# Kernel tuning notes

Measured on AMD Instinct MI355X. Metric: run time of the kernel, lower is better.

Reference implementation:

```python
import jax, jax.numpy as jnp
import numpy as np

B, S, D = 8, 512, 1024
F = 4 * D        # FFN hidden
E = 8            # num experts
SCALE = 0.02


def setup_inputs() -> dict:
    key = jax.random.key(0)
    ks = jax.random.split(key, 16)
    n = lambda k, shape, s=SCALE: (jax.random.normal(k, shape, dtype=jnp.float32) * s)
    task_ids = jax.random.randint(ks[15], (B,), 0, E)
    return {
        "hidden_states": jax.random.normal(ks[0], (B, S, D), dtype=jnp.float32),
        "ohe_task": jax.nn.one_hot(task_ids, E, dtype=jnp.float32),
        # base model (2-layer FFN) params
        "W1": n(ks[1], (D, F)), "b1": n(ks[2], (F,)),
        "W2": n(ks[3], (F, D)), "b2": n(ks[4], (D,)),
        # expert task vectors (expert_sd - base_sd), stacked over experts
        "T_W1": n(ks[5], (E, D, F)), "T_b1": n(ks[6], (E, F)),
        "T_W2": n(ks[7], (E, F, D)), "T_b2": n(ks[8], (E, D)),
        # gate: 2 hidden ReLU layers then linear to E
        "Wg1": n(ks[9], (D, D)), "bg1": jnp.zeros((D,), jnp.float32),
        "Wg2": n(ks[10], (D, D)), "bg2": jnp.zeros((D,), jnp.float32),
        "Wgo": n(ks[11], (D, E)), "bgo": jnp.zeros((E,), jnp.float32),
    }


def reference(hidden_states, ohe_task, W1, b1, W2, b2,
              T_W1, T_b1, T_W2, T_b2,
              Wg1, bg1, Wg2, bg2, Wgo, bgo):
    x = hidden_states  # [B,S,D]
    # --- router: per-token logits -> softmax over experts -> mean over seq ---
    h = jax.nn.relu(jnp.einsum("bsd,de->bse", x, Wg1) + bg1)
    h = jax.nn.relu(jnp.einsum("bsd,de->bse", h, Wg2) + bg2)
    logits = jnp.einsum("bsd,de->bse", h, Wgo) + bgo        # [B,S,E]
    gate_weights = jax.nn.softmax(logits, axis=-1).mean(axis=1)  # [B,E]
    # --- per-sample weighted merge of expert task vectors into base params ---
    coeff = gate_weights + ohe_task                          # [B,E]
    W1b = W1 + jnp.einsum("be,edf->bdf", coeff, T_W1)        # [B,D,F]
    b1b = b1 + coeff @ T_b1                                  # [B,F]
    W2b = W2 + jnp.einsum("be,efd->bfd", coeff, T_W2)        # [B,F,D]
    b2b = b2 + coeff @ T_b2                                  # [B,D]
    # --- batched functional forward through merged FFN ---
    hmid = jax.nn.gelu(jnp.einsum("bsd,bdf->bsf", x, W1b) + b1b[:, None, :],
                       approximate=False)
    out = jnp.einsum("bsf,bfd->bsd", hmid, W2b) + b2b[:, None, :]
    return out, gate_weights
```

## Files before the change

kernel.cpp:

```cpp
#include <hip/hip_runtime.h>
#include <hip/hip_bf16.h>

typedef __attribute__((ext_vector_type(8))) short s16x8;
typedef __attribute__((ext_vector_type(4))) float f32x4;

#define GLOAD_LDS16(gsrc, ldst) \
  __builtin_amdgcn_global_load_lds((const __attribute__((address_space(1))) void*)(gsrc), \
      (__attribute__((address_space(3))) void*)(ldst), 16, 0, 0)

__global__ __launch_bounds__(256) void cvt_bf16(const float* __restrict__ in,
                                                __hip_bfloat16* __restrict__ out, long n) {
  long i = ((long)blockIdx.x * 256 + threadIdx.x) * 4;
  if (i + 3 >= n) return;
  float4 v = *(const float4*)(in + i);
  __hip_bfloat16 tmp[4] = {__float2bfloat16(v.x), __float2bfloat16(v.y),
                           __float2bfloat16(v.z), __float2bfloat16(v.w)};
  *(ushort4*)((unsigned short*)out + i) = *(const ushort4*)tmp;
}

template<int NB>
__global__ __launch_bounds__(256) void merge_transpose(
    const float* __restrict__ Wb, const float* __restrict__ T,
    const float* __restrict__ coeff, __hip_bfloat16* __restrict__ Out,
    int K, int N, int nE) {
  int ntn = N >> 6;
  int k0 = (blockIdx.x / ntn) << 6;
  int n0 = (blockIdx.x % ntn) << 6;
  int t = threadIdx.x;
  long KN = (long)K * N;

  float4 accb[NB][4];
#pragma unroll
  for (int i = 0; i < 4; ++i) {
    int e = i * 256 + t; int kk = e >> 4, nn = (e & 15) << 2;
    float4 bv = *(const float4*)&Wb[(long)(k0 + kk) * N + n0 + nn];
#pragma unroll
    for (int b2 = 0; b2 < NB; ++b2) accb[b2][i] = bv;
  }
  for (int ex = 0; ex < nE; ++ex) {
    float c[NB];
#pragma unroll
    for (int b2 = 0; b2 < NB; ++b2) c[b2] = coeff[b2 * 8 + ex];
#pragma unroll
    for (int i = 0; i < 4; ++i) {
      int e = i * 256 + t; int kk = e >> 4, nn = (e & 15) << 2;
      float4 tv = *(const float4*)&T[(long)ex * KN + (long)(k0 + kk) * N + n0 + nn];
#pragma unroll
      for (int b2 = 0; b2 < NB; ++b2) {
        accb[b2][i].x += c[b2] * tv.x; accb[b2][i].y += c[b2] * tv.y;
        accb[b2][i].z += c[b2] * tv.z; accb[b2][i].w += c[b2] * tv.w;
      }
    }
  }
  __shared__ __hip_bfloat16 lds[64 * 66];
  for (int b2 = 0; b2 < NB; ++b2) {
    __syncthreads();
#pragma unroll
    for (int i = 0; i < 4; ++i) {
      int e = i * 256 + t; int kk = e >> 4, nn = (e & 15) << 2;
      lds[kk * 66 + nn + 0] = __float2bfloat16(accb[b2][i].x);
      lds[kk * 66 + nn + 1] = __float2bfloat16(accb[b2][i].y);
      lds[kk * 66 + nn + 2] = __float2bfloat16(accb[b2][i].z);
      lds[kk * 66 + nn + 3] = __float2bfloat16(accb[b2][i].w);
    }
    __syncthreads();
#pragma unroll
    for (int i = 0; i < 4; ++i) {
      int o = i * 256 + t; int n2 = o >> 4, k2 = (o & 15) << 2;
      __hip_bfloat16 tmp[4];
#pragma unroll
      for (int j = 0; j < 4; ++j) tmp[j] = lds[(k2 + j) * 66 + n2];
      *(ushort4*)((unsigned short*)&Out[(long)b2 * KN + (long)(n0 + n2) * K + k0 + k2]) =
          *(const ushort4*)tmp;
    }
  }
}

__global__ __launch_bounds__(256) void merge_bias(const float* __restrict__ base,
                                                  const float* __restrict__ T,
                                                  const float* __restrict__ coeff,
                                                  float* __restrict__ out, int n) {
  int b = blockIdx.y;
  int i = blockIdx.x * 256 + threadIdx.x;
  if (i >= n) return;
  float v = base[i];
#pragma unroll
  for (int e = 0; e < 8; ++e) v += coeff[b * 8 + e] * T[(long)e * n + i];
  out[(long)b * n + i] = v;
}

template<int ACT, bool OUTBF>
__global__ __launch_bounds__(256, 2) void gemm_bt(
    const __hip_bfloat16* __restrict__ A, const __hip_bfloat16* __restrict__ BT,
    const float* __restrict__ bias, void* __restrict__ Out,
    int N, int K, long sA, long sB, long sBias, long sOut) {
  int bid = blockIdx.x;
  int b = blockIdx.y;
  int m = (bid & 7) * 4 + ((bid >> 3) & 3), n = bid >> 5;
  int m0 = m << 7, n0 = n << 7;

  const __hip_bfloat16* Ab = A + (long)b * sA;
  const __hip_bfloat16* Bb = BT + (long)b * sB;

  __shared__ __align__(16) __hip_bfloat16 As[128 * 64];
  __shared__ __align__(16) __hip_bfloat16 Bs[128 * 64];

  int t = threadIdx.x;
  int lane = t & 63;
  int wid = t >> 6;
  int wm = wid >> 1, wn = wid & 1;
  int lr = lane & 15, kg = lane >> 4;

  f32x4 acc[4][4] = {};

  for (int kt = 0; kt < K; kt += 64) {
#pragma unroll
    for (int is = 0; is < 4; ++is) {
      int ci = is * 256 + t;
      int row = ci >> 3, cpos = ci & 7;
      int csrc = cpos ^ (row & 7);
      GLOAD_LDS16(Ab + (long)(m0 + row) * K + kt + csrc * 8, &As[ci * 8]);
      GLOAD_LDS16(Bb + (long)(n0 + row) * K + kt + csrc * 8, &Bs[ci * 8]);
    }
    __syncthreads();
#pragma unroll
    for (int ks = 0; ks < 2; ++ks) {
      s16x8 af[4], bfr[4];
#pragma unroll
      for (int mi = 0; mi < 4; ++mi) {
        int row = wm * 64 + mi * 16 + lr;
        int c = (ks * 4 + kg) ^ (row & 7);
        af[mi] = *(const s16x8*)&As[row * 64 + c * 8];
      }
#pragma unroll
      for (int ni = 0; ni < 4; ++ni) {
        int row = wn * 64 + ni * 16 + lr;
        int c = (ks * 4 + kg) ^ (row & 7);
        bfr[ni] = *(const s16x8*)&Bs[row * 64 + c * 8];
      }
#pragma unroll
      for (int mi = 0; mi < 4; ++mi)
#pragma unroll
        for (int ni = 0; ni < 4; ++ni)
          acc[mi][ni] = __builtin_amdgcn_mfma_f32_16x16x32_bf16(bfr[ni], af[mi], acc[mi][ni], 0, 0, 0);
    }
    __syncthreads();
  }

#pragma unroll
  for (int mi = 0; mi < 4; ++mi) {
    int row = m0 + wm * 64 + mi * 16 + lr;
#pragma unroll
    for (int ni = 0; ni < 4; ++ni) {
      int colb = n0 + wn * 64 + ni * 16 + kg * 4;
      float bv4[4] = {0.f, 0.f, 0.f, 0.f};
      if (bias != nullptr) {
        float4 bb = *(const float4*)&bias[(long)b * sBias + colb];
        bv4[0] = bb.x; bv4[1] = bb.y; bv4[2] = bb.z; bv4[3] = bb.w;
      }
      float v[4];
#pragma unroll
      for (int j = 0; j < 4; ++j) {
        v[j] = acc[mi][ni][j] + bv4[j];
        if (ACT == 1) v[j] = fmaxf(v[j], 0.f);
        else if (ACT == 2) v[j] = 0.5f * v[j] * (1.f + erff(v[j] * 0.70710678118f));
      }
      long off = (long)b * sOut + (long)row * N + colb;
      if (OUTBF) {
        __hip_bfloat16 tmp[4] = {__float2bfloat16(v[0]), __float2bfloat16(v[1]),
                                 __float2bfloat16(v[2]), __float2bfloat16(v[3])};
        *(ushort4*)((unsigned short*)Out + off) = *(const ushort4*)tmp;
      } else {
        *(float4*)((float*)Out + off) = make_float4(v[0], v[1], v[2], v[3]);
      }
    }
  }
}

template<int ACT, bool OUTBF>
__global__ __launch_bounds__(512, 4) void gemm8w(
    const __hip_bfloat16* __restrict__ A, const __hip_bfloat16* __restrict__ BT,
    const float* __restrict__ bias, void* __restrict__ Out,
    int N, int K, long sA, long sB, long sBias, long sOut,
    int kLen, long ksOut, int mBits, int nBits) {
  int bid = blockIdx.x;
  int b = bid & 7;
  int t2 = bid >> 3;
  int m = t2 & ((1 << mBits) - 1);
  int rest = t2 >> mBits;
  int n = rest & ((1 << nBits) - 1);
  int kc = rest >> nBits;
  int m0 = m << 7, n0 = n << 8;
  int kOff = kc * kLen;

  const __hip_bfloat16* Ab = A + (long)b * sA;
  const __hip_bfloat16* Bb = BT + (long)b * sB;

  __shared__ __align__(16) __hip_bfloat16 As[128 * 64];
  __shared__ __align__(16) __hip_bfloat16 Bs[256 * 64];

  int t = threadIdx.x;
  int lane = t & 63;
  int wid = t >> 6;
  int wm = wid >> 2;
  int wn = wid & 3;
  int lr = lane & 15, kg = lane >> 4;

  f32x4 acc[4][4] = {};

  for (int kt = kOff; kt < kOff + kLen; kt += 64) {
#pragma unroll
    for (int is = 0; is < 2; ++is) {
      int ci = is * 512 + t;
      int row = ci >> 3, cpos = ci & 7;
      int csrc = cpos ^ (row & 7);
      GLOAD_LDS16(Ab + (long)(m0 + row) * K + kt + csrc * 8, &As[ci * 8]);
    }
#pragma unroll
    for (int is = 0; is < 4; ++is) {
      int ci = is * 512 + t;
      int row = ci >> 3, cpos = ci & 7;
      int csrc = cpos ^ (row & 7);
      GLOAD_LDS16(Bb + (long)(n0 + row) * K + kt + csrc * 8, &Bs[ci * 8]);
    }
    __syncthreads();
#pragma unroll
    for (int ks = 0; ks < 2; ++ks) {
      s16x8 af[4], bfr[4];
#pragma unroll
      for (int mi = 0; mi < 4; ++mi) {
        int row = wm * 64 + mi * 16 + lr;
        int c = (ks * 4 + kg) ^ (row & 7);
        af[mi] = *(const s16x8*)&As[row * 64 + c * 8];
      }
#pragma unroll
      for (int ni = 0; ni < 4; ++ni) {
        int row = wn * 64 + ni * 16 + lr;
        int c = (ks * 4 + kg) ^ (row & 7);
        bfr[ni] = *(const s16x8*)&Bs[row * 64 + c * 8];
      }
#pragma unroll
      for (int mi = 0; mi < 4; ++mi)
#pragma unroll
        for (int ni = 0; ni < 4; ++ni)
          acc[mi][ni] = __builtin_amdgcn_mfma_f32_16x16x32_bf16(bfr[ni], af[mi], acc[mi][ni], 0, 0, 0);
    }
    __syncthreads();
  }

#pragma unroll
  for (int mi = 0; mi < 4; ++mi) {
    int row = m0 + wm * 64 + mi * 16 + lr;
#pragma unroll
    for (int ni = 0; ni < 4; ++ni) {
      int colb = n0 + wn * 64 + ni * 16 + kg * 4;
      float bv4[4] = {0.f, 0.f, 0.f, 0.f};
      if (bias != nullptr) {
        float4 bb = *(const float4*)&bias[(long)b * sBias + colb];
        bv4[0] = bb.x; bv4[1] = bb.y; bv4[2] = bb.z; bv4[3] = bb.w;
      }
      float v[4];
#pragma unroll
      for (int j = 0; j < 4; ++j) {
        v[j] = acc[mi][ni][j] + bv4[j];
        if (ACT == 1) v[j] = fmaxf(v[j], 0.f);
        else if (ACT == 2) v[j] = 0.5f * v[j] * (1.f + erff(v[j] * 0.70710678118f));
      }
      long off = kc * ksOut + (long)b * sOut + (long)row * N + colb;
      if (OUTBF) {
        __hip_bfloat16 tmp[4] = {__float2bfloat16(v[0]), __float2bfloat16(v[1]),
                                 __float2bfloat16(v[2]), __float2bfloat16(v[3])};
        *(ushort4*)((unsigned short*)Out + off) = *(const ushort4*)tmp;
      } else {
        *(float4*)((float*)Out + off) = make_float4(v[0], v[1], v[2], v[3]);
      }
    }
  }
}

template<int NP>
__global__ __launch_bounds__(256) void reduceN_bias(
    const __hip_bfloat16* __restrict__ p, const float* __restrict__ b2b,
    float* __restrict__ out, long ksOut) {
  long i = ((long)blockIdx.x * 256 + threadIdx.x) * 8;
  const unsigned short* ps = (const unsigned short*)p;
  int d = (int)(i & 1023);
  int b = (int)(i >> 19);
  const float* bp = b2b + (long)b * 1024 + d;
  float o[8];
#pragma unroll
  for (int j = 0; j < 8; ++j) o[j] = bp[j];
#pragma unroll
  for (int pp = 0; pp < NP; ++pp) {
    ushort4 a0 = *(const ushort4*)(ps + pp * ksOut + i);
    ushort4 a1 = *(const ushort4*)(ps + pp * ksOut + i + 4);
    unsigned short av[8] = {a0.x, a0.y, a0.z, a0.w, a1.x, a1.y, a1.z, a1.w};
#pragma unroll
    for (int j = 0; j < 8; ++j)
      o[j] += __bfloat162float(*(__hip_bfloat16*)&av[j]);
  }
  *(float4*)(out + i) = make_float4(o[0], o[1], o[2], o[3]);
  *(float4*)(out + i + 4) = make_float4(o[4], o[5], o[6], o[7]);
}

__global__ __launch_bounds__(256) void router_logits(
    const __hip_bfloat16* __restrict__ Hg2, const float* __restrict__ Wgo,
    const float* __restrict__ bgo, float* __restrict__ probs) {
  int r = blockIdx.x;
  int t = threadIdx.x;
  float acc[8] = {};
#pragma unroll
  for (int j = 0; j < 4; ++j) {
    int k = j * 256 + t;
    float h = __bfloat162float(Hg2[(long)r * 1024 + k]);
    const float4* wp = (const float4*)&Wgo[k * 8];
    float4 w0 = wp[0], w1 = wp[1];
    acc[0] += h * w0.x; acc[1] += h * w0.y; acc[2] += h * w0.z; acc[3] += h * w0.w;
    acc[4] += h * w1.x; acc[5] += h * w1.y; acc[6] += h * w1.z; acc[7] += h * w1.w;
  }
#pragma unroll
  for (int off = 32; off >= 1; off >>= 1)
#pragma unroll
    for (int e = 0; e < 8; ++e) acc[e] += __shfl_down(acc[e], off);
  __shared__ float lds[4][8];
  int wid = t >> 6, lane = t & 63;
  if (lane == 0)
#pragma unroll
    for (int e = 0; e < 8; ++e) lds[wid][e] = acc[e];
  __syncthreads();
  if (t == 0) {
    float lg[8];
#pragma unroll
    for (int e = 0; e < 8; ++e) lg[e] = lds[0][e] + lds[1][e] + lds[2][e] + lds[3][e] + bgo[e];
    float mx = lg[0];
#pragma unroll
    for (int e = 1; e < 8; ++e) mx = fmaxf(mx, lg[e]);
    float s = 0.f;
#pragma unroll
    for (int e = 0; e < 8; ++e) { lg[e] = __expf(lg[e] - mx); s += lg[e]; }
    float inv = 1.f / s;
#pragma unroll
    for (int e = 0; e < 8; ++e) probs[(long)r * 8 + e] = lg[e] * inv;
  }
}

__global__ __launch_bounds__(256) void router_mean(
    const float* __restrict__ probs, const float* __restrict__ ohe,
    float* __restrict__ gate_out, float* __restrict__ coeff) {
  int b = blockIdx.x;
  int t = threadIdx.x;
  int e = t & 7, sg = t >> 3;
  float s = 0.f;
#pragma unroll
  for (int j = 0; j < 16; ++j)
    s += probs[((long)b * 512 + sg + j * 32) * 8 + e];
  __shared__ float lds[256];
  lds[t] = s;
  __syncthreads();
  if (t < 8) {
    float tot = 0.f;
#pragma unroll
    for (int g = 0; g < 32; ++g) tot += lds[g * 8 + t];
    float gw = tot / 512.f;
    gate_out[b * 8 + t] = gw;
    coeff[b * 8 + t] = gw + ohe[b * 8 + t];
  }
}

extern "C" void kernel_launch(void* const* d_in, const int* in_sizes, int n_in,
                              void* d_out, int out_size, void* d_ws, size_t ws_size,
                              hipStream_t stream) {
  const float* x    = (const float*)d_in[0];
  const float* ohe  = (const float*)d_in[1];
  const float* W1   = (const float*)d_in[2];
  const float* b1   = (const float*)d_in[3];
  const float* W2   = (const float*)d_in[4];
  const float* b2   = (const float*)d_in[5];
  const float* T_W1 = (const float*)d_in[6];
  const float* T_b1 = (const float*)d_in[7];
  const float* T_W2 = (const float*)d_in[8];
  const float* T_b2 = (const float*)d_in[9];
  const float* Wg1  = (const float*)d_in[10];
  const float* bg1  = (const float*)d_in[11];
  const float* Wg2  = (const float*)d_in[12];
  const float* bg2  = (const float*)d_in[13];
  const float* Wgo  = (const float*)d_in[14];
  const float* bgo  = (const float*)d_in[15];
  float* out = (float*)d_out;
  float* gate_out = out + (long)8 * 512 * 1024;

  char* w = (char*)d_ws;
  __hip_bfloat16* xb   = (__hip_bfloat16*)(w);
  __hip_bfloat16* Wg1T = (__hip_bfloat16*)(w + 8388608);
  __hip_bfloat16* Wg2T = (__hip_bfloat16*)(w + 10485760);
  __hip_bfloat16* Hg1  = (__hip_bfloat16*)(w + 12582912);
  __hip_bfloat16* Hg2  = (__hip_bfloat16*)(w + 20971520);
  float*          probs= (float*)(w + 29360128);
  float*          coeff= (float*)(w + 29491200);
  float*          b1b  = (float*)(w + 29492224);
  float*          b2b  = (float*)(w + 29623296);
  __hip_bfloat16* hmid = (__hip_bfloat16*)(w + 29656064);
  __hip_bfloat16* Wb   = (__hip_bfloat16*)(w + 63210496);
  __hip_bfloat16* partR= (__hip_bfloat16*)(w + 130319360);
  bool rich = ws_size >= (size_t)197428224;

  const long SSD = (long)512 * 1024;
  const long SSF = (long)512 * 4096;
  const long OUTN = (long)8 * 512 * 1024;

  cvt_bf16<<<4096, 256, 0, stream>>>(x, xb, (long)8 * 512 * 1024);
  merge_transpose<1><<<16 * 16, 256, 0, stream>>>(Wg1, nullptr, nullptr, Wg1T, 1024, 1024, 0);
  merge_transpose<1><<<16 * 16, 256, 0, stream>>>(Wg2, nullptr, nullptr, Wg2T, 1024, 1024, 0);
  gemm_bt<1, true><<<dim3(256, 1), 256, 0, stream>>>(xb, Wg1T, bg1, Hg1,
      1024, 1024, 0, 0, 0, 0);
  gemm_bt<1, true><<<dim3(256, 1), 256, 0, stream>>>(Hg1, Wg2T, bg2, Hg2,
      1024, 1024, 0, 0, 0, 0);
  router_logits<<<4096, 256, 0, stream>>>(Hg2, Wgo, bgo, probs);
  router_mean<<<8, 256, 0, stream>>>(probs, ohe, gate_out, coeff);
  merge_bias<<<dim3(16, 8), 256, 0, stream>>>(b1, T_b1, coeff, b1b, 4096);
  merge_bias<<<dim3(4, 8), 256, 0, stream>>>(b2, T_b2, coeff, b2b, 1024);
  merge_transpose<8><<<16 * 64, 256, 0, stream>>>(W1, T_W1, coeff, Wb, 1024, 4096, 8);
  gemm8w<2, true><<<dim3(512, 1), 512, 0, stream>>>(xb, Wb, b1b, hmid,
      4096, 1024, SSD, (long)4096 * 1024, 4096, SSF, 1024, 0, 2, 4);
  merge_transpose<8><<<64 * 16, 256, 0, stream>>>(W2, T_W2, coeff, Wb, 4096, 1024, 8);
  if (rich) {
    gemm8w<0, true><<<dim3(512, 1), 512, 0, stream>>>(hmid, Wb, nullptr, partR,
        1024, 4096, SSF, (long)4096 * 1024, 0, SSD, 1024, OUTN, 2, 2);
    reduceN_bias<4><<<2048, 256, 0, stream>>>(partR, b2b, out, OUTN);
  } else {
    __hip_bfloat16* part = xb;
    gemm8w<0, true><<<dim3(256, 1), 512, 0, stream>>>(hmid, Wb, nullptr, part,
        1024, 4096, SSF, (long)4096 * 1024, 0, SSD, 2048, OUTN, 2, 2);
    reduceN_bias<2><<<2048, 256, 0, stream>>>(part, b2b, out, OUTN);
  }
}
```

Before: 260.1 us.

## Split-K first FFN GEMM and fuse reduction with bias and GELU

In the workspace-rich path, the first FFN GEMM now runs split-K over 2 partitions with twice the grid, writing bf16 partials. A new reduce2_gelu kernel sums them, adds the merged bias and applies exact GELU. The second GEMM's split-K depth goes from 4 to 8 partitions, also with a larger grid. The aim is better CU occupancy on the GEMMs, at the cost of extra partial-buffer traffic, an extra launch, and bf16 rounding of the partial sums.

```diff
diff --git a/kernel.cpp b/kernel.cpp
--- a/kernel.cpp
+++ b/kernel.cpp
@@ -301,6 +301,32 @@
   }
   *(float4*)(out + i) = make_float4(o[0], o[1], o[2], o[3]);
   *(float4*)(out + i + 4) = make_float4(o[4], o[5], o[6], o[7]);
+}
+
+__global__ __launch_bounds__(256) void reduce2_gelu(
+    const __hip_bfloat16* __restrict__ p, const float* __restrict__ b1b,
+    __hip_bfloat16* __restrict__ out, long ksOut) {
+  long i = ((long)blockIdx.x * 256 + threadIdx.x) * 8;
+  const unsigned short* ps = (const unsigned short*)p;
+  int d = (int)(i & 4095);
+  int b = (int)(i >> 21);
+  const float* bp = b1b + (long)b * 4096 + d;
+  ushort4 a0 = *(const ushort4*)(ps + i);
+  ushort4 a1 = *(const ushort4*)(ps + i + 4);
+  ushort4 c0 = *(const ushort4*)(ps + ksOut + i);
+  ushort4 c1 = *(const ushort4*)(ps + ksOut + i + 4);
+  unsigned short av[8] = {a0.x, a0.y, a0.z, a0.w, a1.x, a1.y, a1.z, a1.w};
+  unsigned short cv[8] = {c0.x, c0.y, c0.z, c0.w, c1.x, c1.y, c1.z, c1.w};
+  __hip_bfloat16 tmp[8];
+#pragma unroll
+  for (int j = 0; j < 8; ++j) {
+    float v = __bfloat162float(*(__hip_bfloat16*)&av[j]) +
+              __bfloat162float(*(__hip_bfloat16*)&cv[j]) + bp[j];
+    v = 0.5f * v * (1.f + erff(v * 0.70710678118f));
+    tmp[j] = __float2bfloat16(v);
+  }
+  *(ushort4*)((unsigned short*)out + i) = *(const ushort4*)tmp;
+  *(ushort4*)((unsigned short*)out + i + 4) = *(const ushort4*)(tmp + 4);
 }
 
 __global__ __launch_bounds__(256) void router_logits(
@@ -407,6 +433,7 @@
   const long SSD = (long)512 * 1024;
   const long SSF = (long)512 * 4096;
   const long OUTN = (long)8 * 512 * 1024;
+  const long OUTF = (long)8 * 512 * 4096;
 
   cvt_bf16<<<4096, 256, 0, stream>>>(x, xb, (long)8 * 512 * 1024);
   merge_transpose<1><<<16 * 16, 256, 0, stream>>>(Wg1, nullptr, nullptr, Wg1T, 1024, 1024, 0);
@@ -420,14 +447,19 @@
   merge_bias<<<dim3(16, 8), 256, 0, stream>>>(b1, T_b1, coeff, b1b, 4096);
   merge_bias<<<dim3(4, 8), 256, 0, stream>>>(b2, T_b2, coeff, b2b, 1024);
   merge_transpose<8><<<16 * 64, 256, 0, stream>>>(W1, T_W1, coeff, Wb, 1024, 4096, 8);
-  gemm8w<2, true><<<dim3(512, 1), 512, 0, stream>>>(xb, Wb, b1b, hmid,
-      4096, 1024, SSD, (long)4096 * 1024, 4096, SSF, 1024, 0, 2, 4);
-  merge_transpose<8><<<64 * 16, 256, 0, stream>>>(W2, T_W2, coeff, Wb, 4096, 1024, 8);
+
   if (rich) {
-    gemm8w<0, true><<<dim3(512, 1), 512, 0, stream>>>(hmid, Wb, nullptr, partR,
-        1024, 4096, SSF, (long)4096 * 1024, 0, SSD, 1024, OUTN, 2, 2);
-    reduceN_bias<4><<<2048, 256, 0, stream>>>(partR, b2b, out, OUTN);
+    gemm8w<0, true><<<dim3(1024, 1), 512, 0, stream>>>(xb, Wb, nullptr, partR,
+        4096, 1024, SSD, (long)4096 * 1024, 0, SSF, 512, OUTF, 2, 4);
+    reduce2_gelu<<<8192, 256, 0, stream>>>(partR, b1b, hmid, OUTF);
+    merge_transpose<8><<<64 * 16, 256, 0, stream>>>(W2, T_W2, coeff, Wb, 4096, 1024, 8);
+    gemm8w<0, true><<<dim3(1024, 1), 512, 0, stream>>>(hmid, Wb, nullptr, partR,
+        1024, 4096, SSF, (long)4096 * 1024, 0, SSD, 512, OUTN, 2, 2);
+    reduceN_bias<8><<<2048, 256, 0, stream>>>(partR, b2b, out, OUTN);
   } else {
+    gemm8w<2, true><<<dim3(512, 1), 512, 0, stream>>>(xb, Wb, b1b, hmid,
+        4096, 1024, SSD, (long)4096 * 1024, 4096, SSF, 1024, 0, 2, 4);
+    merge_transpose<8><<<64 * 16, 256, 0, stream>>>(W2, T_W2, coeff, Wb, 4096, 1024, 8);
     __hip_bfloat16* part = xb;
     gemm8w<0, true><<<dim3(256, 1), 512, 0, stream>>>(hmid, Wb, nullptr, part,
         1024, 4096, SSF, (long)4096 * 1024, 0, SSD, 2048, OUTN, 2, 2);
```

After: 321.3 us. +23.5%, slower.

## Register-staged double-buffered loads in big GEMMs; split-K gemm_bt for fallback

Applied to the files above, without the earlier changes.

The batched FFN GEMM kernel drops direct global-to-LDS loads. It now prefetches the next K tile into registers while the current tile is computed, then writes it to shared memory, using raw barriers instead of two syncthreads per iteration. This is meant to overlap global memory latency with MFMA work. It also adds a split-K mode to the 128x128 gemm_bt kernel, used for the second FFN GEMM on the low-workspace path. The costs are higher register pressure, and with a single LDS buffer the write of the next tile must wait for a barrier after compute.

```diff
diff --git a/kernel.cpp b/kernel.cpp
--- a/kernel.cpp
+++ b/kernel.cpp
@@ -89,15 +89,18 @@
   out[(long)b * n + i] = v;
 }
 
-template<int ACT, bool OUTBF>
+template<int MODE, int ACT, bool OUTBF>
 __global__ __launch_bounds__(256, 2) void gemm_bt(
     const __hip_bfloat16* __restrict__ A, const __hip_bfloat16* __restrict__ BT,
     const float* __restrict__ bias, void* __restrict__ Out,
-    int N, int K, long sA, long sB, long sBias, long sOut) {
+    int N, int K, long sA, long sB, long sBias, long sOut,
+    int kLen, long ksOut) {
   int bid = blockIdx.x;
-  int b = blockIdx.y;
-  int m = (bid & 7) * 4 + ((bid >> 3) & 3), n = bid >> 5;
+  int b, m, n, kc = 0;
+  if (MODE == 0)      { b = blockIdx.y; m = (bid & 7) * 4 + ((bid >> 3) & 3); n = bid >> 5; }
+  else                { b = bid & 7; int tile = bid >> 3; m = tile & 3; n = (tile >> 2) & 7; kc = tile >> 5; }
   int m0 = m << 7, n0 = n << 7;
+  int kOff = kc * kLen;
 
   const __hip_bfloat16* Ab = A + (long)b * sA;
   const __hip_bfloat16* Bb = BT + (long)b * sB;
@@ -113,7 +116,7 @@
 
   f32x4 acc[4][4] = {};
 
-  for (int kt = 0; kt < K; kt += 64) {
+  for (int kt = kOff; kt < kOff + kLen; kt += 64) {
 #pragma unroll
     for (int is = 0; is < 4; ++is) {
       int ci = is * 256 + t;
@@ -165,7 +168,7 @@
         if (ACT == 1) v[j] = fmaxf(v[j], 0.f);
         else if (ACT == 2) v[j] = 0.5f * v[j] * (1.f + erff(v[j] * 0.70710678118f));
       }
-      long off = (long)b * sOut + (long)row * N + colb;
+      long off = kc * ksOut + (long)b * sOut + (long)row * N + colb;
       if (OUTBF) {
         __hip_bfloat16 tmp[4] = {__float2bfloat16(v[0]), __float2bfloat16(v[1]),
                                  __float2bfloat16(v[2]), __float2bfloat16(v[3])};
@@ -178,7 +181,7 @@
 }
 
 template<int ACT, bool OUTBF>
-__global__ __launch_bounds__(512, 4) void gemm8w(
+__global__ __launch_bounds__(512, 4) void gemm8w_rs(
     const __hip_bfloat16* __restrict__ A, const __hip_bfloat16* __restrict__ BT,
     const float* __restrict__ bias, void* __restrict__ Out,
     int N, int K, long sA, long sB, long sBias, long sOut,
@@ -207,23 +210,31 @@
   int lr = lane & 15, kg = lane >> 4;
 
   f32x4 acc[4][4] = {};
-
-  for (int kt = kOff; kt < kOff + kLen; kt += 64) {
+  s16x8 ra[2], rb[4];
+
+  auto gload = [&](int kt) {
 #pragma unroll
     for (int is = 0; is < 2; ++is) {
       int ci = is * 512 + t;
       int row = ci >> 3, cpos = ci & 7;
       int csrc = cpos ^ (row & 7);
-      GLOAD_LDS16(Ab + (long)(m0 + row) * K + kt + csrc * 8, &As[ci * 8]);
+      ra[is] = *(const s16x8*)(Ab + (long)(m0 + row) * K + kt + csrc * 8);
     }
 #pragma unroll
     for (int is = 0; is < 4; ++is) {
       int ci = is * 512 + t;
       int row = ci >> 3, cpos = ci & 7;
       int csrc = cpos ^ (row & 7);
-      GLOAD_LDS16(Bb + (long)(n0 + row) * K + kt + csrc * 8, &Bs[ci * 8]);
-    }
-    __syncthreads();
+      rb[is] = *(const s16x8*)(Bb + (long)(n0 + row) * K + kt + csrc * 8);
+    }
+  };
+  auto dswrite = [&]() {
+#pragma unroll
+    for (int is = 0; is < 2; ++is) { int ci = is * 512 + t; *(s16x8*)&As[ci * 8] = ra[is]; }
+#pragma unroll
+    for (int is = 0; is < 4; ++is) { int ci = is * 512 + t; *(s16x8*)&Bs[ci * 8] = rb[is]; }
+  };
+  auto compute = [&]() {
 #pragma unroll
     for (int ks = 0; ks < 2; ++ks) {
       s16x8 af[4], bfr[4];
@@ -245,7 +256,23 @@
         for (int ni = 0; ni < 4; ++ni)
           acc[mi][ni] = __builtin_amdgcn_mfma_f32_16x16x32_bf16(bfr[ni], af[mi], acc[mi][ni], 0, 0, 0);
     }
-    __syncthreads();
+  };
+
+  int nk = kLen >> 6;
+  gload(kOff);
+  dswrite();
+  if (nk > 1) gload(kOff + 64);
+  asm volatile("s_waitcnt lgkmcnt(0)" ::: "memory");
+  __builtin_amdgcn_s_barrier();
+  for (int it = 0; it < nk; ++it) {
+    compute();
+    __builtin_amdgcn_s_barrier();
+    if (it + 1 < nk) {
+      dswrite();
+      if (it + 2 < nk) gload(kOff + ((it + 2) << 6));
+      asm volatile("s_waitcnt lgkmcnt(0)" ::: "memory");
+      __builtin_amdgcn_s_barrier();
+    }
   }
 
 #pragma unroll
@@ -411,26 +438,26 @@
   cvt_bf16<<<4096, 256, 0, stream>>>(x, xb, (long)8 * 512 * 1024);
   merge_transpose<1><<<16 * 16, 256, 0, stream>>>(Wg1, nullptr, nullptr, Wg1T, 1024, 1024, 0);
   merge_transpose<1><<<16 * 16, 256, 0, stream>>>(Wg2, nullptr, nullptr, Wg2T, 1024, 1024, 0);
-  gemm_bt<1, true><<<dim3(256, 1), 256, 0, stream>>>(xb, Wg1T, bg1, Hg1,
-      1024, 1024, 0, 0, 0, 0);
-  gemm_bt<1, true><<<dim3(256, 1), 256, 0, stream>>>(Hg1, Wg2T, bg2, Hg2,
-      1024, 1024, 0, 0, 0, 0);
+  gemm_bt<0, 1, true><<<dim3(256, 1), 256, 0, stream>>>(xb, Wg1T, bg1, Hg1,
+      1024, 1024, 0, 0, 0, 0, 1024, 0);
+  gemm_bt<0, 1, true><<<dim3(256, 1), 256, 0, stream>>>(Hg1, Wg2T, bg2, Hg2,
+      1024, 1024, 0, 0, 0, 0, 1024, 0);
   router_logits<<<4096, 256, 0, stream>>>(Hg2, Wgo, bgo, probs);
   router_mean<<<8, 256, 0, stream>>>(probs, ohe, gate_out, coeff);
   merge_bias<<<dim3(16, 8), 256, 0, stream>>>(b1, T_b1, coeff, b1b, 4096);
   merge_bias<<<dim3(4, 8), 256, 0, stream>>>(b2, T_b2, coeff, b2b, 1024);
   merge_transpose<8><<<16 * 64, 256, 0, stream>>>(W1, T_W1, coeff, Wb, 1024, 4096, 8);
-  gemm8w<2, true><<<dim3(512, 1), 512, 0, stream>>>(xb, Wb, b1b, hmid,
+  gemm8w_rs<2, true><<<dim3(512, 1), 512, 0, stream>>>(xb, Wb, b1b, hmid,
       4096, 1024, SSD, (long)4096 * 1024, 4096, SSF, 1024, 0, 2, 4);
   merge_transpose<8><<<64 * 16, 256, 0, stream>>>(W2, T_W2, coeff, Wb, 4096, 1024, 8);
   if (rich) {
-    gemm8w<0, true><<<dim3(512, 1), 512, 0, stream>>>(hmid, Wb, nullptr, partR,
+    gemm8w_rs<0, true><<<dim3(512, 1), 512, 0, stream>>>(hmid, Wb, nullptr, partR,
         1024, 4096, SSF, (long)4096 * 1024, 0, SSD, 1024, OUTN, 2, 2);
     reduceN_bias<4><<<2048, 256, 0, stream>>>(partR, b2b, out, OUTN);
   } else {
     __hip_bfloat16* part = xb;
-    gemm8w<0, true><<<dim3(256, 1), 512, 0, stream>>>(hmid, Wb, nullptr, part,
-        1024, 4096, SSF, (long)4096 * 1024, 0, SSD, 2048, OUTN, 2, 2);
+    gemm_bt<2, 0, true><<<dim3(512, 1), 256, 0, stream>>>(hmid, Wb, nullptr, part,
+        1024, 4096, SSF, (long)4096 * 1024, 0, SSD, 2048, OUTN);
     reduceN_bias<2><<<2048, 256, 0, stream>>>(part, b2b, out, OUTN);
   }
 }
```

Measured after the change: 267.4 us. 2.8% more time.
